# Optimization experiments

Hardware: AMD Instinct MI355X
Metric: run time of the kernel (lower is better)

## Reference

```python
import jax, jax.numpy as jnp
import numpy as np

B, N, DIM, HEAD = 4, 2048, 1024, 16
HD = DIM // HEAD
LN_EPS = 1e-5


def setup_inputs() -> dict:
    key = jax.random.key(0)
    k1, k2, k3, k4 = jax.random.split(key, 4)
    x = jax.random.normal(k1, (B, N, DIM), dtype=jnp.float32)
    A = jax.random.normal(k2, (B, N, HEAD, 1), dtype=jnp.float32)
    ln_w = jnp.ones((DIM,), dtype=jnp.float32)
    ln_b = jnp.zeros((DIM,), dtype=jnp.float32)
    Wqk = jax.random.normal(k3, (2 * DIM, DIM), dtype=jnp.float32) * (DIM ** -0.5)
    wv = jax.random.normal(k4, (1, 1), dtype=jnp.float32)
    return {"x": x, "A": A, "ln_w": ln_w, "ln_b": ln_b, "Wqk": Wqk, "wv": wv}


def reference(x, A, ln_w, ln_b, Wqk, wv):
    b, n, dim = x.shape
    head = A.shape[2]
    hd = dim // head
    scale = dim ** -0.5  # NOTE: source uses full-dim scale, not head_dim

    # LayerNorm
    mu = jnp.mean(x, axis=-1, keepdims=True)
    xc = x - mu
    var = jnp.mean(xc * xc, axis=-1, keepdims=True)
    xn = xc * jax.lax.rsqrt(var + LN_EPS) * ln_w + ln_b

    # QK projection: [B,N,2*dim] -> q,k [B,head,N,hd]
    qk = jnp.einsum('bnd,ed->bne', xn, Wqk)
    qk = qk.reshape(b, n, 2, head, hd)
    q = qk[:, :, 0].transpose(0, 2, 1, 3)  # [B,H,N,hd]
    k = qk[:, :, 1].transpose(0, 2, 1, 3)

    # v = Linear(1,1,bias=False)(A), head-major layout [B,H,N,1]
    v = (A * wv[0, 0]).transpose(0, 2, 1, 3)

    scores = jnp.einsum('bhnd,bhmd->bhnm', q, k) * scale  # [B,H,N,N]
    attn = jax.nn.softmax(scores, axis=-1)
    out = jnp.einsum('bhnm,bhme->bhne', attn, v)  # [B,H,N,1]
    A_plus = out.transpose(0, 2, 1, 3)  # [B,N,H,1]
    return A + A_plus
```

## Files before the change

kernel.cpp:

```cpp
#include <hip/hip_runtime.h>

#define B_    4
#define N_    2048
#define DIM_  1024
#define HEAD_ 16
#define HD_   64
#define M_    (B_*N_)
#define E_    (2*DIM_)

typedef short          frag8 __attribute__((ext_vector_type(8)));
typedef float          facc4 __attribute__((ext_vector_type(4)));
typedef unsigned short ush4  __attribute__((ext_vector_type(4)));
typedef _Float16       hv4   __attribute__((ext_vector_type(4)));
typedef _Float16       hv2   __attribute__((ext_vector_type(2)));

#define AS1 __attribute__((address_space(1)))
#define AS3 __attribute__((address_space(3)))

__device__ __forceinline__ void gld_lds16(const void* g, void* l) {
    __builtin_amdgcn_global_load_lds((AS1 void*)(void*)g, (AS3 void*)l, 16, 0, 0);
}

__device__ __forceinline__ unsigned short f2bf(float f) {
    return __builtin_bit_cast(unsigned short, (__bf16)f);
}

__global__ __launch_bounds__(256) void prep_kernel(const float* __restrict__ x,
                                                   const float* __restrict__ lw,
                                                   const float* __restrict__ lb,
                                                   const float* __restrict__ Wqk,
                                                   const float* __restrict__ A,
                                                   const float* __restrict__ wv,
                                                   unsigned short* __restrict__ xn,
                                                   unsigned short* __restrict__ wb,
                                                   unsigned short* __restrict__ v16) {
    __shared__ float red[8];
    const int bid = blockIdx.x;
    const int t   = threadIdx.x;
    if (bid < M_) {
        const float4 v = ((const float4*)(x + (size_t)bid * DIM_))[t];
        float s  = v.x + v.y + v.z + v.w;
        float sq = v.x*v.x + v.y*v.y + v.z*v.z + v.w*v.w;
#pragma unroll
        for (int off = 32; off > 0; off >>= 1) {
            s  += __shfl_xor(s,  off);
            sq += __shfl_xor(sq, off);
        }
        const int w = t >> 6;
        if ((t & 63) == 0) { red[w] = s; red[4 + w] = sq; }
        __syncthreads();
        s  = red[0] + red[1] + red[2] + red[3];
        sq = red[4] + red[5] + red[6] + red[7];
        const float mu   = s * (1.0f / DIM_);
        const float rstd = rsqrtf(sq * (1.0f / DIM_) - mu * mu + 1e-5f);
        const float4 wv4 = ((const float4*)lw)[t];
        const float4 bv4 = ((const float4*)lb)[t];
        ush4 o;
        o[0] = f2bf((v.x - mu) * rstd * wv4.x + bv4.x);
        o[1] = f2bf((v.y - mu) * rstd * wv4.y + bv4.y);
        o[2] = f2bf((v.z - mu) * rstd * wv4.z + bv4.z);
        o[3] = f2bf((v.w - mu) * rstd * wv4.w + bv4.w);
        *(ush4*)(xn + (size_t)bid * DIM_ + t * 4) = o;
    } else if (bid < M_ + 2048) {
        const int i = (bid - M_) * 256 + t;
        const float4 v = ((const float4*)Wqk)[i];
        ush4 o;
        o[0] = f2bf(v.x); o[1] = f2bf(v.y); o[2] = f2bf(v.z); o[3] = f2bf(v.w);
        ((ush4*)wb)[i] = o;
    } else {
        const int bh = bid - (M_ + 2048);
        const int b = bh >> 4, h = bh & 15;
        const float wvv = wv[0];
#pragma unroll
        for (int i = 0; i < 8; ++i) {
            const int n = i * 256 + t;
            const float f = A[((size_t)(b * N_ + n)) * HEAD_ + h] * wvv;
            v16[(size_t)bh * N_ + n] = __builtin_bit_cast(unsigned short, (_Float16)f);
        }
    }
}

__global__ __launch_bounds__(512, 2) void gemm_qk(const unsigned short* __restrict__ xn,
                                                  const unsigned short* __restrict__ wb,
                                                  unsigned short* __restrict__ qo,
                                                  unsigned short* __restrict__ ko) {
    __shared__ __attribute__((aligned(16))) char lds[131072];
    const int t    = threadIdx.x;
    const int lane = t & 63;
    const int wid  = t >> 6;
    const int wr   = wid >> 2, wc = wid & 3;
    const int lr   = lane & 15, lg = lane >> 4;
    const int bid  = blockIdx.x;
    const int xcd  = bid & 7;
    const int l    = bid >> 3;
    const int bm   = (xcd << 2) | (l & 3);
    const int bn   = l >> 2;
    const int m0   = bm * 256, e0 = bn * 256;

    const int srow = t >> 3;
    const int ss8  = ((t & 7) ^ (srow & 7)) * 8;
    const int wu16 = (t & ~63) * 16;

    facc4 acc[8][4] = {};
    frag8 a[4][2], b[2][2];

#define STG(mat, tile, half) do {                                              \
        const unsigned short* sp_ = (mat) ? wb : xn;                           \
        const int rb_ = (mat) ? e0 : m0;                                       \
        _Pragma("unroll")                                                      \
        for (int l_ = 0; l_ < 2; ++l_)                                         \
            gld_lds16(sp_ + (size_t)(rb_ + (half)*128 + l_*64 + srow) * DIM_   \
                          + (tile)*64 + ss8,                                   \
                      lds + ((tile)&1)*65536 + (mat)*32768 + (half)*16384      \
                          + l_*8192 + wu16);                                   \
    } while (0)

#define LDA(mh) do {                                                           \
        _Pragma("unroll")                                                      \
        for (int mf_ = 0; mf_ < 4; ++mf_) {                                    \
            const int row_ = wr*128 + (mh)*64 + mf_*16 + lr;                   \
            const int sw_  = (row_ & 7) << 4;                                  \
            const char* ab_ = lds + cb*65536;                                  \
            a[mf_][0] = *(const frag8*)(ab_ + row_*128 + ((lg*16) ^ sw_));     \
            a[mf_][1] = *(const frag8*)(ab_ + row_*128 + ((64 + lg*16) ^ sw_));\
        }                                                                      \
    } while (0)

#define LDB(nh) do {                                                           \
        _Pragma("unroll")                                                      \
        for (int nf_ = 0; nf_ < 2; ++nf_) {                                    \
            const int row_ = wc*64 + (nh)*32 + nf_*16 + lr;                    \
            const int sw_  = (row_ & 7) << 4;                                  \
            const char* bb_ = lds + cb*65536 + 32768;                          \
            b[nf_][0] = *(const frag8*)(bb_ + row_*128 + ((lg*16) ^ sw_));     \
            b[nf_][1] = *(const frag8*)(bb_ + row_*128 + ((64 + lg*16) ^ sw_));\
        }                                                                      \
    } while (0)

#define MM(mh, nh) do {                                                        \
        __builtin_amdgcn_s_setprio(1);                                         \
        _Pragma("unroll")                                                      \
        for (int mf_ = 0; mf_ < 4; ++mf_)                                      \
        _Pragma("unroll")                                                      \
        for (int nf_ = 0; nf_ < 2; ++nf_) {                                    \
            acc[(mh)*4+mf_][(nh)*2+nf_] = __builtin_amdgcn_mfma_f32_16x16x32_bf16( \
                a[mf_][0], b[nf_][0], acc[(mh)*4+mf_][(nh)*2+nf_], 0, 0, 0);   \
            acc[(mh)*4+mf_][(nh)*2+nf_] = __builtin_amdgcn_mfma_f32_16x16x32_bf16( \
                a[mf_][1], b[nf_][1], acc[(mh)*4+mf_][(nh)*2+nf_], 0, 0, 0);   \
        }                                                                      \
        __builtin_amdgcn_s_setprio(0);                                         \
    } while (0)

#define PH_SYNC(NW) do {                                                       \
        asm volatile("s_waitcnt vmcnt(" NW ")" ::: "memory");                  \
        __builtin_amdgcn_s_barrier();                                          \
        asm volatile("" ::: "memory");                                         \
    } while (0)
#define PH_BAR() do {                                                          \
        __builtin_amdgcn_s_barrier();                                          \
        asm volatile("" ::: "memory");                                         \
    } while (0)
#define PH_LGKM() do {                                                         \
        asm volatile("s_waitcnt lgkmcnt(0)" ::: "memory");                     \
        __builtin_amdgcn_sched_barrier(0);                                     \
    } while (0)

    STG(0, 0, 0);  STG(1, 0, 0);  STG(0, 0, 1);  STG(1, 0, 1);
    STG(0, 1, 0);  STG(0, 1, 1);  STG(1, 1, 0);

    for (int m = 0; m < 15; ++m) {
        const int cb = m & 1;
        PH_SYNC("8");
        LDA(0); LDB(0);
        STG(1, m + 1, 1);
        PH_LGKM();
        MM(0, 0);
        PH_SYNC("8");
        LDB(1);
        if (m <= 13) STG(0, m + 2, 0);
        PH_LGKM();
        MM(0, 1);
        PH_SYNC("8");
        LDA(1); LDB(0);
        PH_LGKM();
        MM(1, 0);
        PH_SYNC("8");
        LDB(1);
        if (m <= 13) { STG(0, m + 2, 1); STG(1, m + 2, 0); }
        PH_LGKM();
        MM(1, 1);
    }
    {
        const int cb = 1;
        PH_SYNC("2");  LDA(0); LDB(0); PH_LGKM(); MM(0, 0);
        PH_SYNC("0");  LDB(1);         PH_LGKM(); MM(0, 1);
        PH_BAR();      LDA(1); LDB(0); PH_LGKM(); MM(1, 0);
        PH_BAR();      LDB(1);         PH_LGKM(); MM(1, 1);
    }
#undef STG
#undef LDA
#undef LDB
#undef MM
#undef PH_SYNC
#undef PH_BAR
#undef PH_LGKM

    const float QSCALE = 0.03125f * 1.4426950408889634f;
#pragma unroll
    for (int mf8 = 0; mf8 < 8; ++mf8) {
#pragma unroll
        for (int nf4 = 0; nf4 < 4; ++nf4) {
            const int eg = e0 + wc * 64 + nf4 * 16 + lr;
#pragma unroll
            for (int r = 0; r < 4; ++r) {
                const int   mg = m0 + wr * 128 + mf8 * 16 + lg * 4 + r;
                const int   b_  = mg >> 11;
                const int   n  = mg & (N_ - 1);
                const float val = acc[mf8][nf4][r];
                if (eg < DIM_) {
                    const int h = eg >> 6, d = eg & 63;
                    qo[((size_t)((b_ * HEAD_ + h) * N_ + n)) * HD_ + d] = f2bf(val * QSCALE);
                } else {
                    const int e2 = eg - DIM_;
                    const int h = e2 >> 6, d = e2 & 63;
                    ko[((size_t)((b_ * HEAD_ + h) * N_ + n)) * HD_ + d] = f2bf(val);
                }
            }
        }
    }
}

__global__ __launch_bounds__(256) void attn_kernel(const unsigned short* __restrict__ q,
                                                   const unsigned short* __restrict__ kmat,
                                                   const unsigned short* __restrict__ v16,
                                                   float2* __restrict__ part) {
    __shared__ __attribute__((aligned(16))) char KsB[3 * 8192];
    const int t    = threadIdx.x;
    const int lane = t & 63, w = t >> 6;
    const int lr   = lane & 15, lg = lane >> 4;
    const int id    = blockIdx.x;
    const int split = id >> 9;
    const int bh    = (id >> 3) & 63;
    const int qblk  = id & 7;
    const int b     = bh >> 4, h = bh & 15;
    const int q0    = qblk * 256 + w * 64;

    const int row0  = t >> 3;
    const int koff  = row0 * HD_ + (((t & 7) ^ (row0 & 7)) * 8);
    const int wbase = (t & ~63) * 16;
    const int sw    = (lr & 7) << 4;
    const int off_h0 = lr * 128 + ((lg * 16) ^ sw);
    const int off_h1 = lr * 128 + ((64 + lg * 16) ^ sw);

    const unsigned short* qbase = q    + (size_t)bh * N_ * HD_;
    const unsigned short* kfix  = kmat + (size_t)bh * N_ * HD_ + (size_t)split * 512 * HD_;
    const unsigned short* vfix  = v16  + (size_t)bh * N_ + split * 512;

    frag8 qf[4][2];
#pragma unroll
    for (int qt = 0; qt < 4; ++qt) {
#pragma unroll
        for (int hh = 0; hh < 2; ++hh)
            qf[qt][hh] = *(const frag8*)(qbase + (size_t)(q0 + qt * 16 + lr) * HD_ + hh * 32 + lg * 8);
    }

    hv4 sel, one1;
#pragma unroll
    for (int j = 0; j < 4; ++j) {
        sel[j]  = (lr == 0) ? (_Float16)1.f : (_Float16)0.f;
        one1[j] = (lr == 1) ? (_Float16)1.f : (_Float16)0.f;
    }
    const facc4 z4 = {0.f, 0.f, 0.f, 0.f};
    facc4 acc[4] = {};

#define STAGE(c) do {                                                          \
        gld_lds16(kfix + (c) * 64 * HD_ + koff,                                \
                  KsB + ((c) % 3) * 8192 + wbase);                             \
        gld_lds16(kfix + (c) * 64 * HD_ + koff + 2048,                         \
                  KsB + ((c) % 3) * 8192 + 4096 + wbase);                      \
    } while (0)

#define CHUNK(c) do {                                                          \
        __builtin_amdgcn_s_setprio(1);                                         \
        _Pragma("unroll")                                                      \
        for (int ct = 0; ct < 4; ++ct) {                                       \
            const frag8 kf0 = *(const frag8*)(KsB + ((c) % 3) * 8192 + ct * 2048 + off_h0); \
            const frag8 kf1 = *(const frag8*)(KsB + ((c) % 3) * 8192 + ct * 2048 + off_h1); \
            const hv4 vv = *(const hv4*)(vfix + (c) * 64 + ct * 16 + lg * 4);  \
            const hv4 av = vv * sel + one1;                                    \
            _Pragma("unroll")                                                  \
            for (int qt = 0; qt < 4; ++qt) {                                   \
                facc4 s_ = __builtin_amdgcn_mfma_f32_16x16x32_bf16(kf0, qf[qt][0], z4, 0, 0, 0); \
                s_ = __builtin_amdgcn_mfma_f32_16x16x32_bf16(kf1, qf[qt][1], s_, 0, 0, 0); \
                const hv2 p01 = __builtin_bit_cast(hv2,                        \
                    __builtin_amdgcn_cvt_pkrtz(__builtin_amdgcn_exp2f(s_[0]),  \
                                               __builtin_amdgcn_exp2f(s_[1]))); \
                const hv2 p23 = __builtin_bit_cast(hv2,                        \
                    __builtin_amdgcn_cvt_pkrtz(__builtin_amdgcn_exp2f(s_[2]),  \
                                               __builtin_amdgcn_exp2f(s_[3]))); \
                hv4 pb; pb[0] = p01[0]; pb[1] = p01[1]; pb[2] = p23[0]; pb[3] = p23[1]; \
                acc[qt] = __builtin_amdgcn_mfma_f32_16x16x16f16(av, pb, acc[qt], 0, 0, 0); \
            }                                                                  \
        }                                                                      \
        __builtin_amdgcn_s_setprio(0);                                         \
    } while (0)

#define ITER_S(c, Nw) {                                                        \
        asm volatile("s_waitcnt vmcnt(" Nw ")" ::: "memory");                  \
        __builtin_amdgcn_s_barrier();                                          \
        asm volatile("" ::: "memory");                                         \
        STAGE((c) + 2);                                                        \
        CHUNK(c);                                                              \
    }
#define ITER_N(c, Nw) {                                                        \
        asm volatile("s_waitcnt vmcnt(" Nw ")" ::: "memory");                  \
        __builtin_amdgcn_s_barrier();                                          \
        asm volatile("" ::: "memory");                                         \
        CHUNK(c);                                                              \
    }

    STAGE(0);
    STAGE(1);
    ITER_S(0, "2") ITER_S(1, "2") ITER_S(2, "2") ITER_S(3, "2")
    ITER_S(4, "2") ITER_S(5, "2") ITER_N(6, "2") ITER_N(7, "0")

#undef STAGE
#undef CHUNK
#undef ITER_S
#undef ITER_N

    if (lg == 0) {
#pragma unroll
        for (int qt = 0; qt < 4; ++qt) {
            const int row = q0 + qt * 16 + lr;
            float2 pr; pr.x = acc[qt][0]; pr.y = acc[qt][1];
            part[(size_t)split * (M_ * HEAD_) + ((size_t)(b * N_ + row)) * HEAD_ + h] = pr;
        }
    }
}

__global__ __launch_bounds__(256) void reduce_kernel(const float2* __restrict__ part,
                                                     const float* __restrict__ Ain,
                                                     float* __restrict__ outp) {
    const int i = blockIdx.x * 256 + threadIdx.x;
    const float2 p0 = part[i];
    const float2 p1 = part[1 * (M_ * HEAD_) + i];
    const float2 p2 = part[2 * (M_ * HEAD_) + i];
    const float2 p3 = part[3 * (M_ * HEAD_) + i];
    outp[i] = Ain[i] + (p0.x + p1.x + p2.x + p3.x) / (p0.y + p1.y + p2.y + p3.y);
}

extern "C" void kernel_launch(void* const* d_in, const int* in_sizes, int n_in,
                              void* d_out, int out_size, void* d_ws, size_t ws_size,
                              hipStream_t stream) {
    const float* x   = (const float*)d_in[0];
    const float* A   = (const float*)d_in[1];
    const float* lw  = (const float*)d_in[2];
    const float* lb  = (const float*)d_in[3];
    const float* Wqk = (const float*)d_in[4];
    const float* wv  = (const float*)d_in[5];
    float* outp = (float*)d_out;

    char* ws = (char*)d_ws;
    unsigned short* xn  = (unsigned short*)(ws);
    unsigned short* wb  = (unsigned short*)(ws + 16u * 1024 * 1024);
    unsigned short* qb  = (unsigned short*)(ws + 20u * 1024 * 1024);
    unsigned short* kb  = (unsigned short*)(ws + 36u * 1024 * 1024);
    unsigned short* v16 = (unsigned short*)(ws + 52u * 1024 * 1024);
    float2*         part = (float2*)(ws);

    prep_kernel<<<M_ + 2048 + B_ * HEAD_, 256, 0, stream>>>(x, lw, lb, Wqk, A, wv, xn, wb, v16);
    gemm_qk<<<256, 512, 0, stream>>>(xn, wb, qb, kb);
    attn_kernel<<<2048, 256, 0, stream>>>(qb, kb, v16, part);
    reduce_kernel<<<(M_ * HEAD_) / 256, 256, 0, stream>>>(part, A, outp);
}
```

Before: 103.1 us.

## Give each wave a private K ring buffer and drop block barriers

Each wave now streams its own copy of the K tiles into a private 4-slot LDS ring of 16-row subtiles. It waits only on its own vmcnt, so the per-chunk s_barrier disappears. The block index is also remapped so that blocks sharing the same (batch, head, split) land on the same XCD for L2 reuse. The cost is four times the global K traffic per block, since each wave loads all K itself, plus a larger LDS footprint of 32KB.

```diff
diff --git a/kernel.cpp b/kernel.cpp
--- a/kernel.cpp
+++ b/kernel.cpp
@@ -234,27 +234,28 @@
                                                    const unsigned short* __restrict__ kmat,
                                                    const unsigned short* __restrict__ v16,
                                                    float2* __restrict__ part) {
-    __shared__ __attribute__((aligned(16))) char KsB[3 * 8192];
+    __shared__ __attribute__((aligned(16))) char KsB[4 * 8192];
     const int t    = threadIdx.x;
     const int lane = t & 63, w = t >> 6;
     const int lr   = lane & 15, lg = lane >> 4;
-    const int id    = blockIdx.x;
-    const int split = id >> 9;
-    const int bh    = (id >> 3) & 63;
-    const int qblk  = id & 7;
+    const int bid   = blockIdx.x;
+    const int xcd   = bid & 7;
+    const int inner = (bid >> 3) & 31;
+    const int qblk  = bid >> 8;
+    const int s     = xcd * 32 + inner;
+    const int bh    = s >> 2, split = s & 3;
     const int b     = bh >> 4, h = bh & 15;
     const int q0    = qblk * 256 + w * 64;
 
-    const int row0  = t >> 3;
-    const int koff  = row0 * HD_ + (((t & 7) ^ (row0 & 7)) * 8);
-    const int wbase = (t & ~63) * 16;
+    const int koff  = (lane >> 3) * HD_ + (((lane & 7) ^ ((lane >> 3) & 7)) * 8);
     const int sw    = (lr & 7) << 4;
     const int off_h0 = lr * 128 + ((lg * 16) ^ sw);
     const int off_h1 = lr * 128 + ((64 + lg * 16) ^ sw);
+    char* myl = KsB + w * 8192;
 
     const unsigned short* qbase = q    + (size_t)bh * N_ * HD_;
     const unsigned short* kfix  = kmat + (size_t)bh * N_ * HD_ + (size_t)split * 512 * HD_;
-    const unsigned short* vfix  = v16  + (size_t)bh * N_ + split * 512;
+    const unsigned short* vc    = v16  + (size_t)bh * N_ + split * 512;
 
     frag8 qf[4][2];
 #pragma unroll
@@ -273,61 +274,58 @@
     const facc4 z4 = {0.f, 0.f, 0.f, 0.f};
     facc4 acc[4] = {};
 
-#define STAGE(c) do {                                                          \
-        gld_lds16(kfix + (c) * 64 * HD_ + koff,                                \
-                  KsB + ((c) % 3) * 8192 + wbase);                             \
-        gld_lds16(kfix + (c) * 64 * HD_ + koff + 2048,                         \
-                  KsB + ((c) % 3) * 8192 + 4096 + wbase);                      \
-    } while (0)
-
-#define CHUNK(c) do {                                                          \
+#define STAGE(BUF, P) do {                                                     \
+        gld_lds16((P) + koff,       myl + (BUF) * 2048);                       \
+        gld_lds16((P) + 512 + koff, myl + (BUF) * 2048 + 1024);                \
+    } while (0)
+
+#define CHUNK(J) do {                                                          \
+        const frag8 kf0 = *(const frag8*)(myl + (J) * 2048 + off_h0);          \
+        const frag8 kf1 = *(const frag8*)(myl + (J) * 2048 + off_h1);          \
+        const hv4 vv = *(const hv4*)(vc + lg * 4);                             \
+        const hv4 av = vv * sel + one1;                                        \
         __builtin_amdgcn_s_setprio(1);                                         \
         _Pragma("unroll")                                                      \
-        for (int ct = 0; ct < 4; ++ct) {                                       \
-            const frag8 kf0 = *(const frag8*)(KsB + ((c) % 3) * 8192 + ct * 2048 + off_h0); \
-            const frag8 kf1 = *(const frag8*)(KsB + ((c) % 3) * 8192 + ct * 2048 + off_h1); \
-            const hv4 vv = *(const hv4*)(vfix + (c) * 64 + ct * 16 + lg * 4);  \
-            const hv4 av = vv * sel + one1;                                    \
-            _Pragma("unroll")                                                  \
-            for (int qt = 0; qt < 4; ++qt) {                                   \
-                facc4 s_ = __builtin_amdgcn_mfma_f32_16x16x32_bf16(kf0, qf[qt][0], z4, 0, 0, 0); \
-                s_ = __builtin_amdgcn_mfma_f32_16x16x32_bf16(kf1, qf[qt][1], s_, 0, 0, 0); \
-                const hv2 p01 = __builtin_bit_cast(hv2,                        \
-                    __builtin_amdgcn_cvt_pkrtz(__builtin_amdgcn_exp2f(s_[0]),  \
-                                               __builtin_amdgcn_exp2f(s_[1]))); \
-                const hv2 p23 = __builtin_bit_cast(hv2,                        \
-                    __builtin_amdgcn_cvt_pkrtz(__builtin_amdgcn_exp2f(s_[2]),  \
-                                               __builtin_amdgcn_exp2f(s_[3]))); \
-                hv4 pb; pb[0] = p01[0]; pb[1] = p01[1]; pb[2] = p23[0]; pb[3] = p23[1]; \
-                acc[qt] = __builtin_amdgcn_mfma_f32_16x16x16f16(av, pb, acc[qt], 0, 0, 0); \
-            }                                                                  \
+        for (int qt = 0; qt < 4; ++qt) {                                       \
+            facc4 s_ = __builtin_amdgcn_mfma_f32_16x16x32_bf16(kf0, qf[qt][0], z4, 0, 0, 0); \
+            s_ = __builtin_amdgcn_mfma_f32_16x16x32_bf16(kf1, qf[qt][1], s_, 0, 0, 0); \
+            const hv2 p01 = __builtin_bit_cast(hv2,                            \
+                __builtin_amdgcn_cvt_pkrtz(__builtin_amdgcn_exp2f(s_[0]),      \
+                                           __builtin_amdgcn_exp2f(s_[1])));    \
+            const hv2 p23 = __builtin_bit_cast(hv2,                            \
+                __builtin_amdgcn_cvt_pkrtz(__builtin_amdgcn_exp2f(s_[2]),      \
+                                           __builtin_amdgcn_exp2f(s_[3])));    \
+            hv4 pb; pb[0] = p01[0]; pb[1] = p01[1]; pb[2] = p23[0]; pb[3] = p23[1]; \
+            acc[qt] = __builtin_amdgcn_mfma_f32_16x16x16f16(av, pb, acc[qt], 0, 0, 0); \
         }                                                                      \
         __builtin_amdgcn_s_setprio(0);                                         \
-    } while (0)
-
-#define ITER_S(c, Nw) {                                                        \
-        asm volatile("s_waitcnt vmcnt(" Nw ")" ::: "memory");                  \
-        __builtin_amdgcn_s_barrier();                                          \
-        asm volatile("" ::: "memory");                                         \
-        STAGE((c) + 2);                                                        \
-        CHUNK(c);                                                              \
-    }
-#define ITER_N(c, Nw) {                                                        \
-        asm volatile("s_waitcnt vmcnt(" Nw ")" ::: "memory");                  \
-        __builtin_amdgcn_s_barrier();                                          \
-        asm volatile("" ::: "memory");                                         \
-        CHUNK(c);                                                              \
-    }
-
-    STAGE(0);
-    STAGE(1);
-    ITER_S(0, "2") ITER_S(1, "2") ITER_S(2, "2") ITER_S(3, "2")
-    ITER_S(4, "2") ITER_S(5, "2") ITER_N(6, "2") ITER_N(7, "0")
+        vc += 16;                                                              \
+    } while (0)
+
+#define VM(NW) {                                                               \
+        asm volatile("s_waitcnt vmcnt(" NW ")" ::: "memory");                  \
+        __builtin_amdgcn_sched_barrier(0);                                     \
+    }
+
+    STAGE(0, kfix);
+    STAGE(1, kfix + 1024);
+    STAGE(2, kfix + 2048);
+    const unsigned short* kst = kfix + 3 * 1024;
+
+    for (int o = 0; o < 7; ++o) {
+        VM("4") STAGE(3, kst); kst += 1024; CHUNK(0);
+        VM("4") STAGE(0, kst); kst += 1024; CHUNK(1);
+        VM("4") STAGE(1, kst); kst += 1024; CHUNK(2);
+        VM("4") STAGE(2, kst); kst += 1024; CHUNK(3);
+    }
+    VM("4") STAGE(3, kst); CHUNK(0);
+    VM("4") CHUNK(1);
+    VM("2") CHUNK(2);
+    VM("0") CHUNK(3);
 
 #undef STAGE
 #undef CHUNK
-#undef ITER_S
-#undef ITER_N
+#undef VM
 
     if (lg == 0) {
 #pragma unroll
```

Result: slower. 106.2 us (+3.0%).
